# Optimization experiments

Hardware: AMD Instinct MI355X
Metric: run time of the kernel (lower is better)

The kernel has to match this reference:

```python
import jax, jax.numpy as jnp
import numpy as np

CHANNEL = 256
REDUCTION = 4
GAMMA = 0.5
H_BW = 1.0  # kernel bandwidth h


def setup_inputs() -> dict:
    key = jax.random.key(0)
    k_x, k1, k2, k3, k4 = jax.random.split(key, 5)
    c, r = CHANNEL, CHANNEL // REDUCTION
    x = jax.random.normal(k_x, (32, c, 64, 64), dtype=jnp.float32)
    # fc params, stored as [in, out] for y = x @ W + b (matches nn.Linear math)
    w1 = jax.random.normal(k1, (c, r), dtype=jnp.float32) * (1.0 / np.sqrt(c))
    b1 = jax.random.normal(k2, (r,), dtype=jnp.float32) * 0.01
    w2 = jax.random.normal(k3, (r, c), dtype=jnp.float32) * (1.0 / np.sqrt(r))
    b2 = jax.random.normal(k4, (c,), dtype=jnp.float32) * 0.01
    return {"x": x, "w1": w1, "b1": b1, "w2": w2, "b2": b2}


def reference(x, w1, b1, w2, b2):
    b, c, Hh, Ww = x.shape
    xf = x.reshape(b, c, Hh * Ww)                      # [b, c, n]
    sq = jnp.sum(xf * xf, axis=-1)                     # [b, c]
    gram = jnp.einsum('bcn,bdn->bcd', xf, xf)          # [b, c, c]
    # ||x_i - x_j||^2 = |x_i|^2 + |x_j|^2 - 2 x_i.x_j  (clamped for numerics)
    d2 = jnp.maximum(sq[:, :, None] + sq[:, None, :] - 2.0 * gram, 0.0)
    K = jnp.exp(-0.5 * d2 / (H_BW * H_BW))             # gaussian kernel on dist
    density = jnp.sum(K, axis=-1) / c                  # [b, c]
    hid = jax.nn.relu(density @ w1 + b1)               # [b, c//r]
    attn = jax.nn.sigmoid(hid @ w2 + b2)               # [b, c]
    return x * (attn[:, :, None, None] + GAMMA)
```

## Files before the change

### kernel.cpp

```cpp
#include <hip/hip_runtime.h>
#include <hip/hip_bf16.h>
#include <cstdint>
#include <cstddef>

#define BATCH 32
#define CH    256
#define NSP   4096
#define RED   64
#define GAMMA 0.5f
#define NSPLIT 2
#define KSEG  (NSP / NSPLIT)
#define NKT   (KSEG / 64)
#define TILE_ELEMS (128 * 128)
#define SLICE_STRIDE ((size_t)BATCH * 4 * TILE_ELEMS)

typedef float f32x4 __attribute__((ext_vector_type(4)));
typedef short short8 __attribute__((ext_vector_type(8)));

static __device__ inline unsigned short bfu(float f) {
  __hip_bfloat16 h = __float2bfloat16(f);
  return __builtin_bit_cast(unsigned short, h);
}

__global__ __launch_bounds__(512, 1)
void gram_partial_kernel(const float* __restrict__ x, float* __restrict__ gpart) {
  const int bx   = blockIdx.x;
  const int s    = bx & 1;
  const int tile = (bx >> 1) & 3;
  const int b    = bx >> 3;
  const int tr   = tile >> 1;
  const int tc   = tile & 1;
  const int tid  = threadIdx.x;
  const int lane = tid & 63;
  const int wave = tid >> 6;
  const int wr   = wave >> 2;
  const int wc   = wave & 3;

  __shared__ unsigned short lA[128 * 64];
  __shared__ unsigned short lB[128 * 64];

  const int rsub = tid >> 4;
  const int c4   = tid & 15;

  const float* baseA = x + (size_t)(b * CH + tr * 128) * NSP + s * KSEG;
  const float* baseB = x + (size_t)(b * CH + tc * 128) * NSP + s * KSEG;

  f32x4 pa[4], pb[4];
#pragma unroll
  for (int i = 0; i < 4; ++i) {
    int row = i * 32 + rsub;
    pa[i] = *reinterpret_cast<const f32x4*>(baseA + (size_t)row * NSP + c4 * 4);
    pb[i] = *reinterpret_cast<const f32x4*>(baseB + (size_t)row * NSP + c4 * 4);
  }

  f32x4 acc[4][2];
#pragma unroll
  for (int m = 0; m < 4; ++m)
#pragma unroll
    for (int n = 0; n < 2; ++n)
      acc[m][n] = (f32x4){0.f, 0.f, 0.f, 0.f};

  char* cA = (char*)lA;
  char* cB = (char*)lB;

  for (int kt = 0; kt < NKT; ++kt) {
    __syncthreads();
#pragma unroll
    for (int i = 0; i < 4; ++i) {
      int row = i * 32 + rsub;
      int byte = row * 128 + c4 * 8;
      byte ^= (row & 7) << 4;

      uint64_t wa = (uint64_t)bfu(pa[i][0]) | ((uint64_t)bfu(pa[i][1]) << 16) |
                    ((uint64_t)bfu(pa[i][2]) << 32) | ((uint64_t)bfu(pa[i][3]) << 48);
      *reinterpret_cast<uint64_t*>(cA + byte) = wa;

      uint64_t wb = (uint64_t)bfu(pb[i][0]) | ((uint64_t)bfu(pb[i][1]) << 16) |
                    ((uint64_t)bfu(pb[i][2]) << 32) | ((uint64_t)bfu(pb[i][3]) << 48);
      *reinterpret_cast<uint64_t*>(cB + byte) = wb;
    }
    __syncthreads();

    if (kt + 1 < NKT) {
      const float* kA = baseA + (kt + 1) * 64;
      const float* kB = baseB + (kt + 1) * 64;
#pragma unroll
      for (int i = 0; i < 4; ++i) {
        int row = i * 32 + rsub;
        pa[i] = *reinterpret_cast<const f32x4*>(kA + (size_t)row * NSP + c4 * 4);
        pb[i] = *reinterpret_cast<const f32x4*>(kB + (size_t)row * NSP + c4 * 4);
      }
    }

    short8 af[4][2], bff[2][2];
#pragma unroll
    for (int m = 0; m < 4; ++m)
#pragma unroll
      for (int kh = 0; kh < 2; ++kh) {
        int rowa = wr * 64 + m * 16 + (lane & 15);
        int bytea = rowa * 128 + kh * 64 + ((lane >> 4) * 16);
        bytea ^= (rowa & 7) << 4;
        af[m][kh] = *reinterpret_cast<const short8*>(cA + bytea);
      }
#pragma unroll
    for (int n = 0; n < 2; ++n)
#pragma unroll
      for (int kh = 0; kh < 2; ++kh) {
        int rowb = wc * 32 + n * 16 + (lane & 15);
        int byteb = rowb * 128 + kh * 64 + ((lane >> 4) * 16);
        byteb ^= (rowb & 7) << 4;
        bff[n][kh] = *reinterpret_cast<const short8*>(cB + byteb);
      }

#pragma unroll
    for (int m = 0; m < 4; ++m)
#pragma unroll
      for (int n = 0; n < 2; ++n)
#pragma unroll
        for (int kh = 0; kh < 2; ++kh)
          acc[m][n] = __builtin_amdgcn_mfma_f32_16x16x32_bf16(
              af[m][kh], bff[n][kh], acc[m][n], 0, 0, 0);
  }

  float* g = gpart + ((size_t)s * BATCH + b) * 4 * TILE_ELEMS + (size_t)tile * TILE_ELEMS;
#pragma unroll
  for (int m = 0; m < 4; ++m)
#pragma unroll
    for (int n = 0; n < 2; ++n)
#pragma unroll
      for (int r = 0; r < 4; ++r) {
        int row = wr * 64 + m * 16 + ((lane >> 4) * 4 + r);
        int col = wc * 32 + n * 16 + (lane & 15);
        g[row * 128 + col] = acc[m][n][r];
      }
}

__global__ __launch_bounds__(256)
void density_kernel(const float* __restrict__ gpart, float* __restrict__ density) {
  const int blk  = blockIdx.x;
  const int b    = blk >> 2;
  const int rq   = blk & 3;
  const int t    = threadIdx.x;
  const int lane = t & 63;
  const int wave = t >> 6;

  __shared__ float sq[CH];
  {
    int jt = t >> 7, jr = t & 127;
    size_t off = ((size_t)b * 4 + (size_t)jt * 3) * TILE_ELEMS + (size_t)jr * 128 + jr;
    sq[t] = gpart[off] + gpart[off + SLICE_STRIDE];
  }
  __syncthreads();

  const float* gb = gpart + (size_t)b * 4 * TILE_ELEMS;
#pragma unroll 1
  for (int rr = 0; rr < 16; ++rr) {
    int r = rq * 64 + wave * 16 + rr;
    int rt = r >> 7, rrow = r & 127;
    float sqr = sq[r];
    float ssum = 0.f;
#pragma unroll
    for (int cc = 0; cc < 4; ++cc) {
      int j = cc * 64 + lane;
      int jt = j >> 7;
      size_t off = (size_t)(rt * 2 + jt) * TILE_ELEMS + (size_t)rrow * 128 + (j & 127);
      float g = gb[off] + gb[off + SLICE_STRIDE];
      float d2 = fmaxf(sqr + sq[j] - 2.f * g, 0.f);
      ssum += __expf(-0.5f * d2);
    }
    ssum += __shfl_xor(ssum, 1);
    ssum += __shfl_xor(ssum, 2);
    ssum += __shfl_xor(ssum, 4);
    ssum += __shfl_xor(ssum, 8);
    ssum += __shfl_xor(ssum, 16);
    ssum += __shfl_xor(ssum, 32);
    if (lane == 0) density[b * CH + r] = ssum * (1.0f / CH);
  }
}

__global__ __launch_bounds__(256)
void mlp_kernel(const float* __restrict__ density,
                const float* __restrict__ w1, const float* __restrict__ b1,
                const float* __restrict__ w2, const float* __restrict__ b2,
                float* __restrict__ scale) {
  const int b = blockIdx.x;
  const int t = threadIdx.x;
  __shared__ float dens[CH];
  __shared__ float hid[RED];
  dens[t] = density[b * CH + t];
  __syncthreads();
  if (t < RED) {
    float s = b1[t];
    for (int c = 0; c < CH; ++c) s += dens[c] * w1[c * RED + t];
    hid[t] = fmaxf(s, 0.f);
  }
  __syncthreads();
  float s = b2[t];
#pragma unroll
  for (int h = 0; h < RED; ++h) s += hid[h] * w2[h * CH + t];
  scale[b * CH + t] = 1.f / (1.f + __expf(-s)) + GAMMA;
}

__global__ __launch_bounds__(256)
void scale_kernel(const f32x4* __restrict__ x, const float* __restrict__ scale,
                  f32x4* __restrict__ out, int n4) {
  const int stride = gridDim.x * blockDim.x;
  for (int i = blockIdx.x * blockDim.x + threadIdx.x; i < n4; i += stride) {
    float s = scale[i >> 10];
    out[i] = x[i] * s;
  }
}

extern "C" void kernel_launch(void* const* d_in, const int* in_sizes, int n_in,
                              void* d_out, int out_size, void* d_ws, size_t ws_size,
                              hipStream_t stream) {
  const float* x  = (const float*)d_in[0];
  const float* w1 = (const float*)d_in[1];
  const float* b1 = (const float*)d_in[2];
  const float* w2 = (const float*)d_in[3];
  const float* b2 = (const float*)d_in[4];
  float* out = (float*)d_out;

  float* gpart   = (float*)d_ws;
  float* density = gpart + NSPLIT * SLICE_STRIDE;
  float* scale   = density + BATCH * CH;

  gram_partial_kernel<<<dim3(BATCH * 4 * NSPLIT), dim3(512), 0, stream>>>(x, gpart);
  density_kernel<<<dim3(BATCH * 4), dim3(256), 0, stream>>>(gpart, density);
  mlp_kernel<<<dim3(BATCH), dim3(256), 0, stream>>>(density, w1, b1, w2, b2, scale);

  const int n4 = BATCH * CH * NSP / 4;
  scale_kernel<<<dim3(2048), dim3(256), 0, stream>>>(
      (const f32x4*)x, scale, (f32x4*)out, n4);
}
```

Before: 132.8 us.

## Split Gram K-dimension four ways and fuse density with MLP kernel

Raises the K-split of the Gram computation from 2 to 4, so 512 workgroups run instead of 256, and relaxes launch bounds to allow more resident workgroups per CU. The density and MLP kernels are merged into one 1024-thread workgroup per batch, which drops one launch and the density round-trip through global memory. The scale kernel grid is also doubled. In exchange, the partial-sum workspace doubles and density now runs on only 32 workgroups, which may underuse the GPU for that stage.

Result: slower. 148.8 us (+12.1%).

```diff
diff --git a/kernel.cpp b/kernel.cpp
--- a/kernel.cpp
+++ b/kernel.cpp
@@ -8,7 +8,7 @@
 #define NSP   4096
 #define RED   64
 #define GAMMA 0.5f
-#define NSPLIT 2
+#define NSPLIT 4
 #define KSEG  (NSP / NSPLIT)
 #define NKT   (KSEG / 64)
 #define TILE_ELEMS (128 * 128)
@@ -22,12 +22,12 @@
   return __builtin_bit_cast(unsigned short, h);
 }
 
-__global__ __launch_bounds__(512, 1)
+__global__ __launch_bounds__(512, 4)
 void gram_partial_kernel(const float* __restrict__ x, float* __restrict__ gpart) {
   const int bx   = blockIdx.x;
-  const int s    = bx & 1;
-  const int tile = (bx >> 1) & 3;
-  const int b    = bx >> 3;
+  const int s    = bx & 3;
+  const int tile = (bx >> 2) & 3;
+  const int b    = bx >> 4;
   const int tr   = tile >> 1;
   const int tc   = tile & 1;
   const int tid  = threadIdx.x;
@@ -135,27 +135,34 @@
       }
 }
 
-__global__ __launch_bounds__(256)
-void density_kernel(const float* __restrict__ gpart, float* __restrict__ density) {
-  const int blk  = blockIdx.x;
-  const int b    = blk >> 2;
-  const int rq   = blk & 3;
+__global__ __launch_bounds__(1024)
+void density_mlp_kernel(const float* __restrict__ gpart,
+                        const float* __restrict__ w1, const float* __restrict__ b1,
+                        const float* __restrict__ w2, const float* __restrict__ b2,
+                        float* __restrict__ scale) {
+  const int b    = blockIdx.x;
   const int t    = threadIdx.x;
   const int lane = t & 63;
   const int wave = t >> 6;
 
   __shared__ float sq[CH];
-  {
+  __shared__ float dens[CH];
+  __shared__ float hid[RED];
+
+  if (t < CH) {
     int jt = t >> 7, jr = t & 127;
     size_t off = ((size_t)b * 4 + (size_t)jt * 3) * TILE_ELEMS + (size_t)jr * 128 + jr;
-    sq[t] = gpart[off] + gpart[off + SLICE_STRIDE];
+    float v = 0.f;
+#pragma unroll
+    for (int s = 0; s < NSPLIT; ++s) v += gpart[off + (size_t)s * SLICE_STRIDE];
+    sq[t] = v;
   }
   __syncthreads();
 
   const float* gb = gpart + (size_t)b * 4 * TILE_ELEMS;
 #pragma unroll 1
   for (int rr = 0; rr < 16; ++rr) {
-    int r = rq * 64 + wave * 16 + rr;
+    int r = wave * 16 + rr;
     int rt = r >> 7, rrow = r & 127;
     float sqr = sq[r];
     float ssum = 0.f;
@@ -164,7 +171,9 @@
       int j = cc * 64 + lane;
       int jt = j >> 7;
       size_t off = (size_t)(rt * 2 + jt) * TILE_ELEMS + (size_t)rrow * 128 + (j & 127);
-      float g = gb[off] + gb[off + SLICE_STRIDE];
+      float g = 0.f;
+#pragma unroll
+      for (int s = 0; s < NSPLIT; ++s) g += gb[off + (size_t)s * SLICE_STRIDE];
       float d2 = fmaxf(sqr + sq[j] - 2.f * g, 0.f);
       ssum += __expf(-0.5f * d2);
     }
@@ -174,31 +183,24 @@
     ssum += __shfl_xor(ssum, 8);
     ssum += __shfl_xor(ssum, 16);
     ssum += __shfl_xor(ssum, 32);
-    if (lane == 0) density[b * CH + r] = ssum * (1.0f / CH);
-  }
-}
-
-__global__ __launch_bounds__(256)
-void mlp_kernel(const float* __restrict__ density,
-                const float* __restrict__ w1, const float* __restrict__ b1,
-                const float* __restrict__ w2, const float* __restrict__ b2,
-                float* __restrict__ scale) {
-  const int b = blockIdx.x;
-  const int t = threadIdx.x;
-  __shared__ float dens[CH];
-  __shared__ float hid[RED];
-  dens[t] = density[b * CH + t];
+    if (lane == 0) dens[r] = ssum * (1.0f / CH);
+  }
   __syncthreads();
+
   if (t < RED) {
     float s = b1[t];
+#pragma unroll 4
     for (int c = 0; c < CH; ++c) s += dens[c] * w1[c * RED + t];
     hid[t] = fmaxf(s, 0.f);
   }
   __syncthreads();
-  float s = b2[t];
-#pragma unroll
-  for (int h = 0; h < RED; ++h) s += hid[h] * w2[h * CH + t];
-  scale[b * CH + t] = 1.f / (1.f + __expf(-s)) + GAMMA;
+
+  if (t < CH) {
+    float s = b2[t];
+#pragma unroll
+    for (int h = 0; h < RED; ++h) s += hid[h] * w2[h * CH + t];
+    scale[b * CH + t] = 1.f / (1.f + __expf(-s)) + GAMMA;
+  }
 }
 
 __global__ __launch_bounds__(256)
@@ -221,15 +223,13 @@
   const float* b2 = (const float*)d_in[4];
   float* out = (float*)d_out;
 
-  float* gpart   = (float*)d_ws;
-  float* density = gpart + NSPLIT * SLICE_STRIDE;
-  float* scale   = density + BATCH * CH;
+  float* gpart = (float*)d_ws;
+  float* scale = gpart + NSPLIT * SLICE_STRIDE;
 
   gram_partial_kernel<<<dim3(BATCH * 4 * NSPLIT), dim3(512), 0, stream>>>(x, gpart);
-  density_kernel<<<dim3(BATCH * 4), dim3(256), 0, stream>>>(gpart, density);
-  mlp_kernel<<<dim3(BATCH), dim3(256), 0, stream>>>(density, w1, b1, w2, b2, scale);
+  density_mlp_kernel<<<dim3(BATCH), dim3(1024), 0, stream>>>(gpart, w1, b1, w2, b2, scale);
 
   const int n4 = BATCH * CH * NSP / 4;
-  scale_kernel<<<dim3(2048), dim3(256), 0, stream>>>(
+  scale_kernel<<<dim3(4096), dim3(256), 0, stream>>>(
       (const f32x4*)x, scale, (f32x4*)out, n4);
 }
```
